# Optimization experiments

Hardware: AMD Instinct MI355X
Metric: run time of the kernel (lower is better)

## Reference

```python
import jax, jax.numpy as jnp
import numpy as np

B, T, NF, C, H, TOPK = 4, 8, 8192, 384, 12, 32
D = C // H
SCALE = D ** -0.5  # qk_scale=None -> head_dim**-0.5


def setup_inputs() -> dict:
    key = jax.random.key(0)
    ks = jax.random.split(key, 4)
    x = jax.random.normal(ks[0], (B, T + NF, C), jnp.float32)
    qs_w = jax.random.normal(ks[1], (T, C, C), jnp.float32) * (C ** -0.5)
    kv_w = jax.random.normal(ks[2], (C, 2 * C), jnp.float32) * (C ** -0.5)
    experts_w = jax.random.normal(ks[3], (T, C, C), jnp.float32) * (C ** -0.5)
    return {"x": x, "qs_w": qs_w, "kv_w": kv_w, "experts_w": experts_w}


def reference(x, qs_w, kv_w, experts_w):
    # x: [B, T+NF, C]; first T tokens are task tokens, rest are feature tokens
    feature = x[:, T:, :]                                          # [B,NF,C]
    kv = (feature @ kv_w).reshape(B, NF, 2, H, D)                  # out dim splits [2,H,D]
    k = kv[:, :, 0].transpose(0, 2, 1, 3)                          # [B,H,NF,D]
    v = kv[:, :, 1].transpose(0, 2, 1, 3)                          # [B,H,NF,D]
    # per-task query linears (no bias), one task token each
    q = jnp.einsum('btc,tco->bto', x[:, :T, :], qs_w)              # [B,T,C]
    q = q.reshape(B, T, H, D).transpose(0, 2, 1, 3)                # [B,H,T,D]
    attn = jnp.einsum('bhtd,bhnd->bhtn', q, k) * SCALE             # [B,H,T,NF]
    vals, idx = jax.lax.top_k(attn, TOPK)                          # [B,H,T,K]
    w = jax.nn.softmax(vals, axis=-1)                              # softmax over top-k only
    # attn_token = (scatter(topk softmax) @ v) == weighted gather of v rows
    v_g = jnp.take_along_axis(v[:, :, None], idx[..., None], axis=3)   # [B,H,T,K,D]
    attn_token = jnp.einsum('bhtk,bhtkd->bhtd', w, v_g)
    attn_token = attn_token.transpose(0, 2, 1, 3).reshape(B, T, C)     # [B,T,C]
    # gather raw feature tokens at top-k indices, weight, scatter into padded zeros
    fm = feature.reshape(B, NF, H, D).transpose(0, 2, 1, 3)        # [B,H,NF,D]
    f_g = jnp.take_along_axis(fm[:, :, None], idx[..., None], axis=3) * w[..., None]  # [B,H,T,K,D]
    bi = jnp.arange(B)[:, None, None, None]
    hi = jnp.arange(H)[None, :, None, None]
    ti = jnp.arange(T)[None, None, :, None]
    # topk indices are unique per row -> set is well-defined
    feature_pad = jnp.zeros((B, H, T, NF, D), x.dtype).at[bi, hi, ti, idx].set(f_g)
    feature_pad = feature_pad.transpose(0, 2, 3, 1, 4).reshape(B, T, NF, C)  # [B,T,NF,C]
    # per-task expert linears; einsum with ones weight == sum over tasks
    feature_out = jnp.einsum('btnc,tco->bno', feature_pad, experts_w)  # [B,NF,C]
    token_out = jnp.einsum('btc,tco->bto', attn_token, experts_w)      # [B,T,C]
    return jnp.concatenate([token_out, feature_out], axis=1)          # [B,T+NF,C]
```

## Files before the change

### kernel.cpp

```cpp
#include <hip/hip_runtime.h>
#include <hip/hip_bf16.h>
#include <math.h>

#define B 4
#define T 8
#define NF 8192
#define C 384
#define H 12
#define TOPK 32
#define D 32
#define STOT (T + NF)
#define R (H * T)
#define KSEL 48
#define NCH 4
#define CHSZ (NF / NCH)
#define SCALE 0.17677669529663687f

typedef unsigned int uint;
typedef unsigned short ushort;
typedef short bf16x8 __attribute__((ext_vector_type(8)));
typedef float f32x4 __attribute__((ext_vector_type(4)));

__device__ __forceinline__ ushort bf16u(float a) {
  return __builtin_bit_cast(ushort, __float2bfloat16(a));
}
__device__ __forceinline__ ushort f32_key(float s) {
  uint kb = bf16u(s);
  kb ^= (kb & 0x8000u) ? 0xFFFFu : 0x8000u;
  return (ushort)kb;
}

__global__ __launch_bounds__(256) void ta_qproj_kernel(
    const float* __restrict__ x, const float* __restrict__ qs_w,
    float* __restrict__ q_part) {
  int t = blockIdx.x;
  int o0 = blockIdx.y * 64;
  int z = blockIdx.z;
  int tid = threadIdx.x;
  int o = tid & 63, ks = tid >> 6;
  __shared__ float xs[B][192];
  __shared__ float part[4][B][64];
  if (tid < 192) {
    int b = tid / 48, j4 = (tid % 48) * 4;
    *reinterpret_cast<float4*>(&xs[b][j4]) =
        *reinterpret_cast<const float4*>(x + ((size_t)b * STOT + t) * C + z * 192 + j4);
  }
  __syncthreads();
  float a0 = 0.f, a1 = 0.f, a2 = 0.f, a3 = 0.f;
  const float* w = qs_w + (size_t)t * C * C + (size_t)(z * 192 + ks * 48) * C + o0 + o;
#pragma unroll 8
  for (int c = 0; c < 48; ++c) {
    float wv = w[(size_t)c * C];
    int cj = ks * 48 + c;
    a0 += xs[0][cj] * wv;
    a1 += xs[1][cj] * wv;
    a2 += xs[2][cj] * wv;
    a3 += xs[3][cj] * wv;
  }
  part[ks][0][o] = a0; part[ks][1][o] = a1;
  part[ks][2][o] = a2; part[ks][3][o] = a3;
  __syncthreads();
  {
    int b = tid >> 6, oo = tid & 63;
    float s = part[0][b][oo] + part[1][b][oo] + part[2][b][oo] + part[3][b][oo];
    q_part[(((size_t)z * B + b) * T + t) * C + o0 + oo] = s;
  }
}

__global__ __launch_bounds__(384) void ta_fold_kernel(
    const float* __restrict__ q_part, const float* __restrict__ kv_w,
    float* __restrict__ qk_f32, ushort* __restrict__ qk_bf) {
  int b = blockIdx.x / H, h = blockIdx.x % H;
  int tid = threadIdx.x;
  __shared__ float kS[C][33];
  __shared__ float qh[T][D];
  if (tid < T * D) {
    int t = tid >> 5, d = tid & 31;
    qh[t][d] = q_part[((size_t)b * T + t) * C + h * D + d] +
               q_part[(((size_t)B + b) * T + t) * C + h * D + d];
  }
  for (int j = tid; j < C * 8; j += 384) {
    int c = j >> 3, d4 = (j & 7) * 4;
    float4 v = *reinterpret_cast<const float4*>(
        kv_w + (size_t)c * (2 * C) + h * D + d4);
    kS[c][d4 + 0] = v.x; kS[c][d4 + 1] = v.y;
    kS[c][d4 + 2] = v.z; kS[c][d4 + 3] = v.w;
  }
  __syncthreads();
  float acc[T] = {0.f, 0.f, 0.f, 0.f, 0.f, 0.f, 0.f, 0.f};
#pragma unroll
  for (int d = 0; d < D; ++d) {
    float kv = kS[tid][d];
#pragma unroll
    for (int t = 0; t < T; ++t) acc[t] += qh[t][d] * kv;
  }
#pragma unroll
  for (int t = 0; t < T; ++t) {
    size_t off = ((size_t)b * R + (size_t)h * T + t) * C + tid;
    float a = acc[t];
    qk_f32[off] = a;
    qk_bf[off] = bf16u(a);
  }
}

__global__ __launch_bounds__(256) void ta_scores_kernel(
    const float* __restrict__ x, const ushort* __restrict__ qk_bf,
    ushort* __restrict__ keys, float4* __restrict__ out4) {
  int b = blockIdx.y;
  int n0 = blockIdx.x * 64;
  int tid = threadIdx.x;
  int lane = tid & 63, w = tid >> 6;
  int row16 = lane & 15, kg = lane >> 4;
  __shared__ ushort fS[64][72];
  __shared__ ushort qS[96][72];
  f32x4 acc[6];
#pragma unroll
  for (int i = 0; i < 6; ++i) acc[i] = (f32x4){0.f, 0.f, 0.f, 0.f};

  {
    const int SL = (B * STOT * C / 4) / 512;
    int zbid = blockIdx.y * gridDim.x + blockIdx.x;
    float4 z = {0.f, 0.f, 0.f, 0.f};
    float4* dst = out4 + (size_t)zbid * SL;
    for (int j = tid; j < SL; j += 256) dst[j] = z;
  }

  const float* xb = x + ((size_t)b * STOT + T + n0) * C;
  const ushort* qb = qk_bf + (size_t)b * R * C;

  int frow = tid >> 2, fcg = (tid & 3) * 8;

#pragma unroll 1
  for (int c0 = 0; c0 < C; c0 += 32) {
    {
      const float* src = xb + (size_t)frow * C + c0 + fcg;
      float4 v0 = *reinterpret_cast<const float4*>(src);
      float4 v1 = *reinterpret_cast<const float4*>(src + 4);
      uint4 p;
      p.x = (uint)bf16u(v0.x) | ((uint)bf16u(v0.y) << 16);
      p.y = (uint)bf16u(v0.z) | ((uint)bf16u(v0.w) << 16);
      p.z = (uint)bf16u(v1.x) | ((uint)bf16u(v1.y) << 16);
      p.w = (uint)bf16u(v1.z) | ((uint)bf16u(v1.w) << 16);
      *reinterpret_cast<uint4*>(&fS[frow][fcg]) = p;
    }
#pragma unroll
    for (int s = 0; s < 2; ++s) {
      int u = tid + 256 * s;
      if (u < 384) {
        int row = u >> 2, cg = (u & 3) * 8;
        uint4 v = *reinterpret_cast<const uint4*>(qb + (size_t)row * C + c0 + cg);
        *reinterpret_cast<uint4*>(&qS[row][cg]) = v;
      }
    }
    __syncthreads();
    bf16x8 bfr = *reinterpret_cast<const bf16x8*>(&fS[w * 16 + row16][kg * 8]);
#pragma unroll
    for (int i = 0; i < 6; ++i) {
      bf16x8 afr = *reinterpret_cast<const bf16x8*>(&qS[i * 16 + row16][kg * 8]);
      acc[i] = __builtin_amdgcn_mfma_f32_16x16x32_bf16(afr, bfr, acc[i], 0, 0, 0);
    }
    __syncthreads();
  }
  int n = n0 + w * 16 + row16;
#pragma unroll
  for (int i = 0; i < 6; ++i) {
    int rbase = i * 16 + kg * 4;
#pragma unroll
    for (int reg = 0; reg < 4; ++reg) {
      keys[((size_t)b * R + rbase + reg) * NF + n] = f32_key(acc[i][reg] * SCALE);
    }
  }
}

__global__ __launch_bounds__(256) void ta_selchunk_kernel(
    const ushort* __restrict__ keys, uint* __restrict__ cand_buf) {
  int ch = blockIdx.x, rr = blockIdx.y;
  int tid = threadIdx.x;
  int lane = tid & 63, wvi = tid >> 6;
  __shared__ uint hist[4096];
  __shared__ uint cand[CHSZ];
  __shared__ uint wtot[4];
  __shared__ uint sh_piv, cnt;
  const ushort* kp = keys + (size_t)rr * NF + (size_t)ch * CHSZ;

  {
    uint4 z4 = {0u, 0u, 0u, 0u};
    uint4* hz = reinterpret_cast<uint4*>(hist);
    for (int i = tid; i < 1024; i += 256) hz[i] = z4;
  }
  if (tid == 0) cnt = 0;
  __syncthreads();
  for (int i = tid; i < CHSZ; i += 256) atomicAdd(&hist[kp[i] >> 4], 1u);
  __syncthreads();

  uint pp = 0;
#pragma unroll
  for (int j = 0; j < 16; ++j) pp += hist[tid * 16 + j];
  uint suf = pp;
#pragma unroll
  for (int off = 1; off < 64; off <<= 1) {
    uint o = __shfl_down(suf, off);
    if (lane + off < 64) suf += o;
  }
  if (lane == 0) wtot[wvi] = suf;
  __syncthreads();
  {
    uint later = 0;
    for (int wq = wvi + 1; wq < 4; ++wq) later += wtot[wq];
    uint geg = later + suf;
    uint gng = geg - pp;
    if (geg >= (uint)KSEL && gng < (uint)KSEL) {
      uint run = gng;
      int pv = 0;
      for (int j = 15; j >= 0; --j) {
        uint c = hist[tid * 16 + j];
        uint nrun = run + c;
        if (nrun >= (uint)KSEL && run < (uint)KSEL) pv = tid * 16 + j;
        run = nrun;
      }
      sh_piv = (uint)pv;
    }
  }
  __syncthreads();
  uint piv = sh_piv;
  for (int i = tid; i < CHSZ; i += 256) {
    uint u = kp[i];
    if ((u >> 4) >= piv) {
      uint s = atomicAdd(&cnt, 1u);
      cand[s] = (u << 13) | (8191u - (uint)(ch * CHSZ + i));
    }
  }
  __syncthreads();
  uint m = cnt;
  for (int i2 = tid; i2 < (int)m; i2 += 256) {
    uint me = cand[i2];
    int r = 0;
    for (uint e = 0; e < m; ++e) r += (cand[e] > me);
    if (r < KSEL) cand_buf[((size_t)rr * NCH + ch) * KSEL + r] = me;
  }
}

__global__ __launch_bounds__(384) void ta_merge_kernel(
    const uint* __restrict__ cand_buf, const float* __restrict__ x,
    const float* __restrict__ qk_f32, float* __restrict__ w_buf,
    int* __restrict__ idx_buf) {
  constexpr int M = NCH * KSEL;
  int rr = blockIdx.x;
  int b = rr / R;
  int tid = threadIdx.x;
  __shared__ uint candS[M];
  __shared__ int il[KSEL];
  __shared__ float sv[KSEL];
  __shared__ int rkS[KSEL];
  __shared__ float qS[C];
  __shared__ float smax, esum;

  if (tid < M) candS[tid] = cand_buf[(size_t)rr * M + tid];
  qS[tid] = qk_f32[(size_t)rr * C + tid];
  __syncthreads();
  if (tid < M) {
    uint me = candS[tid];
    int r = 0;
#pragma unroll 8
    for (int e = 0; e < M; ++e) r += (candS[e] > me);
    if (r < KSEL) il[r] = 8191 - (int)(me & 8191u);
  }
  __syncthreads();

  {
    int k = tid >> 3, j = tid & 7;
    const float* fp = x + ((size_t)b * STOT + T + il[k]) * C + j;
    float s = 0.f;
#pragma unroll 8
    for (int m2 = 0; m2 < 48; ++m2) s += fp[m2 * 8] * qS[j + m2 * 8];
    s += __shfl_down(s, 4);
    s += __shfl_down(s, 2);
    s += __shfl_down(s, 1);
    if (j == 0) sv[k] = s * SCALE;
  }
  __syncthreads();
  if (tid < KSEL) {
    float mys = sv[tid];
    int myn = il[tid];
    int r = 0;
#pragma unroll
    for (int e = 0; e < KSEL; ++e) {
      float se = sv[e];
      r += (se > mys) || (se == mys && il[e] < myn);
    }
    rkS[tid] = r;
    if (r == 0) smax = mys;
  }
  __syncthreads();
  float e = 0.f;
  if (tid < KSEL && rkS[tid] < TOPK) e = expf(sv[tid] - smax);
  if (tid < 64) {
    float t2 = e;
#pragma unroll
    for (int off = 32; off; off >>= 1) t2 += __shfl_down(t2, off);
    if (tid == 0) esum = t2;
  }
  __syncthreads();
  if (tid < KSEL && rkS[tid] < TOPK) {
    w_buf[(size_t)rr * TOPK + rkS[tid]] = e / esum;
    idx_buf[(size_t)rr * TOPK + rkS[tid]] = il[tid];
  }
}

__global__ __launch_bounds__(384) void ta_tail_kernel(
    const float* __restrict__ x, const float* __restrict__ kv_w,
    const float* __restrict__ ew, const float* __restrict__ w_buf,
    const int* __restrict__ idx_buf, float* __restrict__ out) {
  constexpr int KQ = TOPK / 4;
  int q = blockIdx.x & 3, rr = blockIdx.x >> 2;
  int t = rr % T, h = (rr / T) % H, b = rr / R;
  int hD = h * D;
  int tid = threadIdx.x;
  __shared__ float wl[KQ];
  __shared__ int il[KQ];
  __shared__ float fbarS[C];
  __shared__ float gS[KQ][D];
  __shared__ float part[8][D];
  __shared__ __align__(16) float attS[D];

  if (tid < KQ) {
    wl[tid] = w_buf[(size_t)rr * TOPK + q * KQ + tid];
    il[tid] = idx_buf[(size_t)rr * TOPK + q * KQ + tid];
  }
  __syncthreads();

  {
    float fbar = 0.f;
    bool ing = (tid >= hD) && (tid < hD + D);
#pragma unroll
    for (int k = 0; k < KQ; ++k) {
      float v = x[((size_t)b * STOT + T + il[k]) * C + tid];
      float wv = wl[k] * v;
      fbar += wv;
      if (ing) gS[k][tid - hD] = wv;
    }
    fbarS[tid] = fbar;
  }
  __syncthreads();

  if (tid < 256) {
    int d = tid & 31, seg = tid >> 5;
    const float* vw = kv_w + C + hD + d;
    float a0 = 0.f, a1 = 0.f;
    int cb = seg * 48;
#pragma unroll 8
    for (int c = 0; c < 48; c += 2) {
      a0 += fbarS[cb + c] * vw[(size_t)(cb + c) * (2 * C)];
      a1 += fbarS[cb + c + 1] * vw[(size_t)(cb + c + 1) * (2 * C)];
    }
    part[seg][d] = a0 + a1;
  }
  __syncthreads();
  if (tid < D) {
    float a = 0.f;
#pragma unroll
    for (int s = 0; s < 8; ++s) a += part[s][tid];
    attS[tid] = a;
  }
  __syncthreads();

  float ewc[D];
  const float* ewt = ew + (size_t)t * C * C + (size_t)hD * C + tid;
#pragma unroll
  for (int dd = 0; dd < D; ++dd) ewc[dd] = ewt[(size_t)dd * C];
  size_t obase = (size_t)b * STOT * C + tid;
#pragma unroll 1
  for (int kk = 0; kk < KQ; ++kk) {
    float y = 0.f;
#pragma unroll
    for (int d4 = 0; d4 < D; d4 += 4) {
      float4 g4 = *reinterpret_cast<const float4*>(&gS[kk][d4]);
      y += g4.x * ewc[d4] + g4.y * ewc[d4 + 1] +
           g4.z * ewc[d4 + 2] + g4.w * ewc[d4 + 3];
    }
    atomicAdd(&out[obase + (size_t)(T + il[kk]) * C], y);
  }
  {
    float y = 0.f;
#pragma unroll
    for (int d4 = 0; d4 < D; d4 += 4) {
      float4 a4 = *reinterpret_cast<const float4*>(attS + d4);
      y += a4.x * ewc[d4] + a4.y * ewc[d4 + 1] +
           a4.z * ewc[d4 + 2] + a4.w * ewc[d4 + 3];
    }
    atomicAdd(&out[obase + (size_t)t * C], y);
  }
}

extern "C" void kernel_launch(void* const* d_in, const int* in_sizes, int n_in,
                              void* d_out, int out_size, void* d_ws, size_t ws_size,
                              hipStream_t stream) {
  const float* x = (const float*)d_in[0];
  const float* qs_w = (const float*)d_in[1];
  const float* kv_w = (const float*)d_in[2];
  const float* ew = (const float*)d_in[3];
  float* out = (float*)d_out;

  char* p = (char*)d_ws;
  float* qk_f32 = (float*)p;  p += (size_t)B * R * C * 4;
  ushort* qk_bf = (ushort*)p; p += (size_t)B * R * C * 2;
  ushort* keys = (ushort*)p;  p += (size_t)B * R * NF * 2;
  uint* cand_buf = (uint*)p;  p += (size_t)B * R * NCH * KSEL * 4;
  float* w_buf = (float*)p;   p += (size_t)B * R * TOPK * 4;
  int* idx_buf = (int*)p;     p += (size_t)B * R * TOPK * 4;
  float* q_part = (float*)p;

  dim3 gq(T, C / 64, 2);
  ta_qproj_kernel<<<gq, 256, 0, stream>>>(x, qs_w, q_part);
  ta_fold_kernel<<<B * H, 384, 0, stream>>>(q_part, kv_w, qk_f32, qk_bf);
  dim3 g2(NF / 64, B);
  ta_scores_kernel<<<g2, 256, 0, stream>>>(x, qk_bf, keys, (float4*)out);
  dim3 gs(NCH, B * R);
  ta_selchunk_kernel<<<gs, 256, 0, stream>>>(keys, cand_buf);
  ta_merge_kernel<<<B * R, 384, 0, stream>>>(cand_buf, x, qk_f32, w_buf, idx_buf);
  ta_tail_kernel<<<4 * B * R, 384, 0, stream>>>(x, kv_w, ew, w_buf, idx_buf, out);
}
```

Baseline: 84.54 us.

## Fuse chunk selection and merge via last-block-done atomic counter

```diff
diff --git a/kernel.cpp b/kernel.cpp
--- a/kernel.cpp
+++ b/kernel.cpp
@@ -172,15 +172,27 @@
   }
 }
 
-__global__ __launch_bounds__(256) void ta_selchunk_kernel(
-    const ushort* __restrict__ keys, uint* __restrict__ cand_buf) {
+__global__ __launch_bounds__(256) void ta_selmerge_kernel(
+    const ushort* __restrict__ keys, const float* __restrict__ x,
+    const float* __restrict__ qk_f32, uint* __restrict__ cand_buf,
+    uint* __restrict__ done, float* __restrict__ w_buf,
+    int* __restrict__ idx_buf) {
+  constexpr int M = NCH * KSEL;
   int ch = blockIdx.x, rr = blockIdx.y;
+  int b = rr / R;
   int tid = threadIdx.x;
   int lane = tid & 63, wvi = tid >> 6;
   __shared__ uint hist[4096];
   __shared__ uint cand[CHSZ];
   __shared__ uint wtot[4];
-  __shared__ uint sh_piv, cnt;
+  __shared__ uint sh_piv, cnt, amlast;
+  __shared__ uint candS[M];
+  __shared__ int il[KSEL];
+  __shared__ float sv[KSEL];
+  __shared__ int rkS[KSEL];
+  __shared__ float qS[C];
+  __shared__ float smax, esum;
+
   const ushort* kp = keys + (size_t)rr * NF + (size_t)ch * CHSZ;
 
   {
@@ -238,25 +250,14 @@
     for (uint e = 0; e < m; ++e) r += (cand[e] > me);
     if (r < KSEL) cand_buf[((size_t)rr * NCH + ch) * KSEL + r] = me;
   }
-}
-
-__global__ __launch_bounds__(384) void ta_merge_kernel(
-    const uint* __restrict__ cand_buf, const float* __restrict__ x,
-    const float* __restrict__ qk_f32, float* __restrict__ w_buf,
-    int* __restrict__ idx_buf) {
-  constexpr int M = NCH * KSEL;
-  int rr = blockIdx.x;
-  int b = rr / R;
-  int tid = threadIdx.x;
-  __shared__ uint candS[M];
-  __shared__ int il[KSEL];
-  __shared__ float sv[KSEL];
-  __shared__ int rkS[KSEL];
-  __shared__ float qS[C];
-  __shared__ float smax, esum;
+  __threadfence();
+  if (tid == 0) amlast = (atomicAdd(&done[rr], 1u) == NCH - 1) ? 1u : 0u;
+  __syncthreads();
+  if (!amlast) return;
+  __threadfence();
 
   if (tid < M) candS[tid] = cand_buf[(size_t)rr * M + tid];
-  qS[tid] = qk_f32[(size_t)rr * C + tid];
+  for (int j = tid; j < C; j += 256) qS[j] = qk_f32[(size_t)rr * C + j];
   __syncthreads();
   if (tid < M) {
     uint me = candS[tid];
@@ -266,7 +267,6 @@
     if (r < KSEL) il[r] = 8191 - (int)(me & 8191u);
   }
   __syncthreads();
-
   {
     int k = tid >> 3, j = tid & 7;
     const float* fp = x + ((size_t)b * STOT + T + il[k]) * C + j;
@@ -278,6 +278,17 @@
     s += __shfl_down(s, 1);
     if (j == 0) sv[k] = s * SCALE;
   }
+  if (tid < 128) {
+    int k = 32 + (tid >> 3), j = tid & 7;
+    const float* fp = x + ((size_t)b * STOT + T + il[k]) * C + j;
+    float s = 0.f;
+#pragma unroll 8
+    for (int m2 = 0; m2 < 48; ++m2) s += fp[m2 * 8] * qS[j + m2 * 8];
+    s += __shfl_down(s, 4);
+    s += __shfl_down(s, 2);
+    s += __shfl_down(s, 1);
+    if (j == 0) sv[k] = s * SCALE;
+  }
   __syncthreads();
   if (tid < KSEL) {
     float mys = sv[tid];
@@ -292,18 +303,20 @@
     if (r == 0) smax = mys;
   }
   __syncthreads();
-  float e = 0.f;
-  if (tid < KSEL && rkS[tid] < TOPK) e = expf(sv[tid] - smax);
-  if (tid < 64) {
-    float t2 = e;
-#pragma unroll
-    for (int off = 32; off; off >>= 1) t2 += __shfl_down(t2, off);
-    if (tid == 0) esum = t2;
-  }
-  __syncthreads();
-  if (tid < KSEL && rkS[tid] < TOPK) {
-    w_buf[(size_t)rr * TOPK + rkS[tid]] = e / esum;
-    idx_buf[(size_t)rr * TOPK + rkS[tid]] = il[tid];
+  {
+    float e = 0.f;
+    if (tid < KSEL && rkS[tid] < TOPK) e = expf(sv[tid] - smax);
+    if (tid < 64) {
+      float t2 = e;
+#pragma unroll
+      for (int off = 32; off; off >>= 1) t2 += __shfl_down(t2, off);
+      if (tid == 0) esum = t2;
+    }
+    __syncthreads();
+    if (tid < KSEL && rkS[tid] < TOPK) {
+      w_buf[(size_t)rr * TOPK + rkS[tid]] = e / esum;
+      idx_buf[(size_t)rr * TOPK + rkS[tid]] = il[tid];
+    }
   }
 }
 
@@ -408,15 +421,17 @@
   uint* cand_buf = (uint*)p;  p += (size_t)B * R * NCH * KSEL * 4;
   float* w_buf = (float*)p;   p += (size_t)B * R * TOPK * 4;
   int* idx_buf = (int*)p;     p += (size_t)B * R * TOPK * 4;
+  uint* done = (uint*)p;      p += (size_t)B * R * 4;
   float* q_part = (float*)p;
 
+  hipMemsetAsync(done, 0, (size_t)B * R * 4, stream);
   dim3 gq(T, C / 64, 2);
   ta_qproj_kernel<<<gq, 256, 0, stream>>>(x, qs_w, q_part);
   ta_fold_kernel<<<B * H, 384, 0, stream>>>(q_part, kv_w, qk_f32, qk_bf);
   dim3 g2(NF / 64, B);
   ta_scores_kernel<<<g2, 256, 0, stream>>>(x, qk_bf, keys, (float4*)out);
   dim3 gs(NCH, B * R);
-  ta_selchunk_kernel<<<gs, 256, 0, stream>>>(keys, cand_buf);
-  ta_merge_kernel<<<B * R, 384, 0, stream>>>(cand_buf, x, qk_f32, w_buf, idx_buf);
+  ta_selmerge_kernel<<<gs, 256, 0, stream>>>(keys, x, qk_f32, cand_buf, done,
+                                             w_buf, idx_buf);
   ta_tail_kernel<<<4 * B * R, 384, 0, stream>>>(x, kv_w, ew, w_buf, idx_buf, out);
 }
```

After: 261.4 us. 209% more time.
